# Performance work log

Measured on AMD Instinct MI355X. Metric: run time of the kernel, lower is better.

Reference implementation:

```python
import jax, jax.numpy as jnp
import numpy as np
import math

B, S, D, H = 4, 1024, 1024, 16
DK = D // H


def setup_inputs() -> dict:
    key = jax.random.key(0)
    ks = jax.random.split(key, 14)
    inp = {
        "query": jax.random.normal(ks[0], (B, S, D), dtype=jnp.float32),
        "key": jax.random.normal(ks[1], (B, S, D), dtype=jnp.float32),
        "value": jax.random.normal(ks[2], (B, S, D), dtype=jnp.float32),
        "attention_bias": jax.random.normal(ks[3], (B, S, S, H), dtype=jnp.float32),
        "mask": jax.random.randint(ks[4], (B, S), 0, 2).astype(bool),
    }
    scale = 0.02
    inp["Wq"] = jax.random.normal(ks[5], (D, D), dtype=jnp.float32) * scale
    inp["bq"] = jnp.zeros((D,), dtype=jnp.float32)
    inp["Wk"] = jax.random.normal(ks[6], (D, D), dtype=jnp.float32) * scale
    inp["bk"] = jnp.zeros((D,), dtype=jnp.float32)
    inp["Wv"] = jax.random.normal(ks[7], (D, D), dtype=jnp.float32) * scale
    inp["bv"] = jnp.zeros((D,), dtype=jnp.float32)
    inp["Wo"] = jax.random.normal(ks[8], (D, D), dtype=jnp.float32) * scale
    inp["bo"] = jnp.zeros((D,), dtype=jnp.float32)
    return inp


def reference(query, key, value, attention_bias, mask, Wq, bq, Wk, bk, Wv, bv, Wo, bo):
    # projections (torch Linear: x @ W.T + b), split heads -> [B,H,S,DK]
    def proj(x, W, b):
        y = x @ W.T + b
        return y.reshape(B, S, H, DK).transpose(0, 2, 1, 3)

    q = proj(query, Wq, bq)
    k = proj(key, Wk, bk)
    v = proj(value, Wv, bv)

    bias = attention_bias.transpose(0, 3, 1, 2)  # [B,H,S,S]
    scores = (jnp.einsum("bhqd,bhkd->bhqk", q, k) + bias) / math.sqrt(DK)

    # pairwise mask: outer product of per-token mask, broadcast over heads
    pm = (mask[:, None, :, None] & mask[:, None, None, :])  # [B,1,S,S]
    scores = jnp.where(pm, scores, jnp.float32(-1e9))

    p_attn = jax.nn.softmax(scores, axis=-1)  # dropout is identity in eval
    x = jnp.einsum("bhqk,bhkd->bhqd", p_attn, v)
    x = x.transpose(0, 2, 1, 3).reshape(B, S, D)
    return x @ Wo.T + bo
```

## Files before the change

### kernel.cpp

```cpp
#include <hip/hip_runtime.h>
#include <hip/hip_bf16.h>
#include <math.h>

#define B_ 4
#define S_ 1024
#define D_ 1024
#define H_ 16
#define DK_ 64

typedef short bf16x8 __attribute__((ext_vector_type(8)));
typedef float f32x4 __attribute__((ext_vector_type(4)));

#define MFMA(a, b, c) __builtin_amdgcn_mfma_f32_16x16x32_bf16(a, b, c, 0, 0, 0)

#define GLDS(gp, lp)                                                        \
    __builtin_amdgcn_global_load_lds(                                       \
        (const __attribute__((address_space(1))) void*)(const void*)(gp),   \
        (__attribute__((address_space(3))) void*)(void*)(lp), 16, 0, 0)

static __device__ __forceinline__ unsigned short f2bf(float f) {
    __hip_bfloat16 h = __float2bfloat16(f);
    return *reinterpret_cast<unsigned short*>(&h);
}
static __device__ __forceinline__ float bf2f(unsigned short u) {
    unsigned int x = ((unsigned int)u) << 16;
    union { unsigned int i; float f; } c; c.i = x; return c.f;
}

__global__ __launch_bounds__(256) void cvt_all(
    const float* __restrict__ a, const float* __restrict__ b, const float* __restrict__ c,
    const float* __restrict__ wa, const float* __restrict__ wb,
    const float* __restrict__ wc, const float* __restrict__ wd,
    unsigned short* __restrict__ oa, unsigned short* __restrict__ ob, unsigned short* __restrict__ oc,
    unsigned short* __restrict__ owa, unsigned short* __restrict__ owb,
    unsigned short* __restrict__ owc, unsigned short* __restrict__ owd)
{
    int bx = blockIdx.x;
    const float* in; unsigned short* out; int i;
    if (bx < 12288) {
        int which = bx >> 12;
        in  = which == 0 ? a : which == 1 ? b : c;
        out = which == 0 ? oa : which == 1 ? ob : oc;
        i = (bx & 4095) * 256 + threadIdx.x;
    } else {
        int b2 = bx - 12288;
        int which = b2 >> 10;
        in  = which == 0 ? wa : which == 1 ? wb : which == 2 ? wc : wd;
        out = which == 0 ? owa : which == 1 ? owb : which == 2 ? owc : owd;
        i = (b2 & 1023) * 256 + threadIdx.x;
    }
    float4 v = ((const float4*)in)[i];
    ushort4 o;
    o.x = f2bf(v.x); o.y = f2bf(v.y); o.z = f2bf(v.z); o.w = f2bf(v.w);
    ((ushort4*)out)[i] = o;
}

__global__ __launch_bounds__(256) void prep_bias(
    const float* __restrict__ bias, const int* __restrict__ mask,
    unsigned short* __restrict__ biasP)
{
    const int t = threadIdx.x;
    const int h = t & 15, u = t >> 4;
    const int x = blockIdx.x;
    const int kt = x & 15, q16 = (x >> 4) & 63, b = x >> 10;

    const unsigned short NEG = f2bf(-28672.f);

    int mk[4];
    #pragma unroll
    for (int j = 0; j < 4; ++j) mk[j] = mask[b * 1024 + kt * 64 + j * 16 + u];

    const float* bb = bias + (((size_t)(b * 1024 + q16 * 16) * 1024) + kt * 64) * 16 + h;
    unsigned short* ob = biasP + ((((size_t)(b * 16 + h) * 64 + q16) * 16 + kt) * 64) * 16;

    #pragma unroll
    for (int quad = 0; quad < 4; ++quad) {
        bf16x8 v0, v1;
        #pragma unroll
        for (int r = 0; r < 4; ++r) {
            int q = quad * 4 + r;
            int mq = mask[b * 1024 + q16 * 16 + q];
            #pragma unroll
            for (int j = 0; j < 4; ++j) {
                float v = bb[((size_t)q * 1024 + j * 16 + u) * 16];
                unsigned short pv = (mq && mk[j]) ? f2bf(v * 0.125f) : NEG;
                if (j < 2) v0[j * 4 + r] = (short)pv;
                else       v1[(j - 2) * 4 + r] = (short)pv;
            }
        }
        unsigned short* dst = ob + (size_t)(quad * 16 + u) * 16;
        *(bf16x8*)(dst) = v0;
        *(bf16x8*)(dst + 8) = v1;
    }
}

__global__ __launch_bounds__(256, 2) void gemm128(
    const unsigned short* __restrict__ X0, const unsigned short* __restrict__ X1,
    const unsigned short* __restrict__ X2,
    const unsigned short* __restrict__ W0, const unsigned short* __restrict__ W1,
    const unsigned short* __restrict__ W2,
    const float* __restrict__ bv0, const float* __restrict__ bv1,
    const float* __restrict__ bv2,
    unsigned short* __restrict__ Y0, unsigned short* __restrict__ Y1,
    unsigned short* __restrict__ Y2,
    const int* __restrict__ mask)
{
    __shared__ unsigned short As[128 * 32];
    __shared__ unsigned short Bs[128 * 32];

    const int z = blockIdx.z;
    const unsigned short* X = z == 0 ? X0 : z == 1 ? X1 : X2;
    const unsigned short* W = z == 0 ? W0 : z == 1 ? W1 : W2;
    const float* bvec = z == 0 ? bv0 : z == 1 ? bv1 : bv2;
    unsigned short* Y = z == 0 ? Y0 : z == 1 ? Y1 : Y2;

    const int t = threadIdx.x;
    const int w = t >> 6, l = t & 63;
    const int lane16 = l & 15, quad = l >> 4;
    const int m0 = blockIdx.y * 128, n0 = blockIdx.x * 128;
    const int wr = w >> 1, wc = w & 1;

    const int srow = w * 16 + (l >> 2);
    const unsigned short* agp = X + (size_t)(m0 + srow) * 1024 + (l & 3) * 8;
    const unsigned short* bgp = W + (size_t)(n0 + srow) * 1024 + (l & 3) * 8;
    unsigned short* alp = As + w * 512 + l * 8;
    unsigned short* blp = Bs + w * 512 + l * 8;

    f32x4 zero = {0.f, 0.f, 0.f, 0.f};
    f32x4 acc[4][4];
    #pragma unroll
    for (int i = 0; i < 4; ++i)
        #pragma unroll
        for (int j = 0; j < 4; ++j) acc[i][j] = zero;

    for (int kt = 0; kt < 1024; kt += 32) {
        GLDS(agp + kt, alp);
        GLDS(agp + kt + 64 * 1024, alp + 2048);
        GLDS(bgp + kt, blp);
        GLDS(bgp + kt + 64 * 1024, blp + 2048);
        __syncthreads();

        bf16x8 af[4], bfv[4];
        #pragma unroll
        for (int i = 0; i < 4; ++i)
            af[i] = *(const bf16x8*)(As + (wr * 64 + i * 16 + lane16) * 32 + quad * 8);
        #pragma unroll
        for (int j = 0; j < 4; ++j)
            bfv[j] = *(const bf16x8*)(Bs + (wc * 64 + j * 16 + lane16) * 32 + quad * 8);

        #pragma unroll
        for (int i = 0; i < 4; ++i)
            #pragma unroll
            for (int j = 0; j < 4; ++j)
                acc[i][j] = MFMA(af[i], bfv[j], acc[i][j]);
        __syncthreads();
    }

    float bvl[4];
    #pragma unroll
    for (int j = 0; j < 4; ++j) bvl[j] = bvec[n0 + wc * 64 + j * 16 + lane16];

    if (z == 2) {
        const int bb = m0 >> 10;
        const int sb = (m0 & 1023) + wr * 64;
        #pragma unroll
        for (int i = 0; i < 4; ++i) {
            #pragma unroll
            for (int j = 0; j < 4; ++j) {
                int n = n0 + wc * 64 + j * 16 + lane16;
                ushort4 pk;
                pk.x = f2bf(acc[i][j][0] + bvl[j]);
                pk.y = f2bf(acc[i][j][1] + bvl[j]);
                pk.z = f2bf(acc[i][j][2] + bvl[j]);
                pk.w = f2bf(acc[i][j][3] + bvl[j]);
                int s = sb + i * 16 + quad * 4;
                *(ushort4*)(Y + ((size_t)(bb * 1024 + n)) * 1024 + s) = pk;
            }
        }
    } else {
        #pragma unroll
        for (int i = 0; i < 4; ++i) {
            int mrow[4];
            #pragma unroll
            for (int r = 0; r < 4; ++r)
                mrow[r] = (z == 0) ? mask[m0 + wr * 64 + i * 16 + quad * 4 + r] : 1;
            #pragma unroll
            for (int j = 0; j < 4; ++j) {
                int n = n0 + wc * 64 + j * 16 + lane16;
                #pragma unroll
                for (int r = 0; r < 4; ++r) {
                    size_t m = m0 + wr * 64 + i * 16 + quad * 4 + r;
                    float val = acc[i][j][r] + bvl[j];
                    if (z == 0) val = mrow[r] ? val * 0.125f : 0.f;
                    Y[m * 1024 + n] = f2bf(val);
                }
            }
        }
    }
}

__global__ __launch_bounds__(256, 2) void attn_mfma(
    const unsigned short* __restrict__ Qp, const unsigned short* __restrict__ Kp,
    const unsigned short* __restrict__ VpT, const unsigned short* __restrict__ biasP,
    unsigned short* __restrict__ Xp)
{
    __shared__ unsigned short Ks[2][64 * 64];
    __shared__ unsigned short Vs[2][64 * 64];
    __shared__ unsigned short Ps[4][16 * 64];

    const int t = threadIdx.x;
    const int w = t >> 6, l = t & 63;
    const int lane16 = l & 15, quad = l >> 4;

    const int bid = blockIdx.x;
    const int bh = bid & 63, qt = bid >> 6;
    const int h = bh & 15, b = bh >> 4;
    const int qrow0 = qt * 64 + w * 16;
    const int q16 = qt * 4 + w;

    bf16x8 qf[2];
    #pragma unroll
    for (int c = 0; c < 2; ++c)
        qf[c] = *(const bf16x8*)(Qp + (size_t)(b * 1024 + qrow0 + lane16) * 1024
                                 + h * 64 + c * 32 + quad * 8);

    bf16x8 ones;
    #pragma unroll
    for (int e = 0; e < 8; ++e) ones[e] = (short)0x3F80;

    const unsigned short* bp = biasP
        + ((((size_t)(b * 16 + h) * 64 + q16) * 16) * 64 + l) * 16;

    const int krow = w * 8 + (l >> 3);
    const int kgran = (l & 7) ^ ((l >> 3) & 7);
    const unsigned short* kg = Kp + (size_t)(b * 1024 + krow) * 1024 + h * 64 + kgran * 8;
    const unsigned short* vg = VpT + ((size_t)(b * 16 + h) * 64 + krow) * 1024 + kgran * 8;
    unsigned short* kst = &Ks[0][w * 512 + l * 8];
    unsigned short* vst = &Vs[0][w * 512 + l * 8];

    GLDS(kg, kst);
    GLDS(kg + (size_t)32 * 1024, kst + 32 * 64);
    GLDS(vg, vst);
    GLDS(vg + (size_t)32 * 1024, vst + 32 * 64);
    bf16x8 bfr0 = *(const bf16x8*)(bp);
    bf16x8 bfr1 = *(const bf16x8*)(bp + 8);

    f32x4 zero = {0.f, 0.f, 0.f, 0.f};
    f32x4 o[4];
    #pragma unroll
    for (int j = 0; j < 4; ++j) o[j] = zero;
    float m_i[4] = {-1e30f, -1e30f, -1e30f, -1e30f};
    float l_i[4] = {0.f, 0.f, 0.f, 0.f};

    char* psb = (char*)&Ps[w][0];

    for (int kt16 = 0; kt16 < 16; ++kt16) {
        const int cur = kt16 & 1;
        __syncthreads();

        if (kt16 < 15) {
            const size_t kn = (size_t)(kt16 + 1) * 64;
            unsigned short* kd = kst + (cur ^ 1) * 4096;
            unsigned short* vd = vst + (cur ^ 1) * 4096;
            GLDS(kg + kn * 1024, kd);
            GLDS(kg + (kn + 32) * 1024, kd + 32 * 64);
            GLDS(vg + kn, vd);
            GLDS(vg + kn + (size_t)32 * 1024, vd + 32 * 64);
        }

        const unsigned short* Kc = &Ks[0][0] + cur * 4096;
        const unsigned short* Vc = &Vs[0][0] + cur * 4096;

        f32x4 s[4];
        #pragma unroll
        for (int j = 0; j < 2; ++j)
            #pragma unroll
            for (int r = 0; r < 4; ++r) {
                s[j][r]     = bf2f((unsigned short)bfr0[j * 4 + r]);
                s[2 + j][r] = bf2f((unsigned short)bfr1[j * 4 + r]);
            }

        __builtin_amdgcn_s_setprio(1);
        #pragma unroll
        for (int j = 0; j < 4; ++j) {
            #pragma unroll
            for (int c = 0; c < 2; ++c) {
                bf16x8 kf = *(const bf16x8*)(Kc + (j * 16 + lane16) * 64
                                             + (((c * 4 + quad) ^ (lane16 & 7)) * 8));
                s[j] = MFMA(qf[c], kf, s[j]);
            }
        }
        __builtin_amdgcn_s_setprio(0);

        if (kt16 < 15) {
            bfr0 = *(const bf16x8*)(bp + (size_t)(kt16 + 1) * 1024);
            bfr1 = *(const bf16x8*)(bp + (size_t)(kt16 + 1) * 1024 + 8);
        }

        float p[4][4];
        float alpha_r[4];
        #pragma unroll
        for (int r = 0; r < 4; ++r) {
            float mx = fmaxf(fmaxf(s[0][r], s[1][r]), fmaxf(s[2][r], s[3][r]));
            #pragma unroll
            for (int d = 1; d < 16; d <<= 1) mx = fmaxf(mx, __shfl_xor(mx, d, 64));
            float mnew = fmaxf(m_i[r], mx);
            float alpha = __expf(m_i[r] - mnew);
            m_i[r] = mnew;
            alpha_r[r] = alpha;
            #pragma unroll
            for (int j = 0; j < 4; ++j) p[j][r] = __expf(s[j][r] - mnew);
            #pragma unroll
            for (int jd = 0; jd < 4; ++jd) o[jd][r] *= alpha;
        }

        #pragma unroll
        for (int j = 0; j < 4; ++j)
            #pragma unroll
            for (int r = 0; r < 4; ++r) {
                int row = quad * 4 + r;
                int cb = (j * 16 + lane16) * 2;
                *(unsigned short*)(psb + row * 128 + (cb ^ ((row & 7) << 4))) = f2bf(p[j][r]);
            }
        asm volatile("" ::: "memory");

        bf16x8 pf[2];
        #pragma unroll
        for (int c = 0; c < 2; ++c) {
            int cb = c * 64 + quad * 16;
            pf[c] = *(const bf16x8*)(psb + lane16 * 128 + (cb ^ ((lane16 & 7) << 4)));
        }

        f32x4 lacc = zero;
        __builtin_amdgcn_s_setprio(1);
        #pragma unroll
        for (int jd = 0; jd < 4; ++jd)
            #pragma unroll
            for (int c = 0; c < 2; ++c) {
                bf16x8 vf = *(const bf16x8*)(Vc + (jd * 16 + lane16) * 64
                                             + (((c * 4 + quad) ^ (lane16 & 7)) * 8));
                o[jd] = MFMA(pf[c], vf, o[jd]);
            }
        #pragma unroll
        for (int c = 0; c < 2; ++c)
            lacc = MFMA(pf[c], ones, lacc);
        __builtin_amdgcn_s_setprio(0);

        #pragma unroll
        for (int r = 0; r < 4; ++r)
            l_i[r] = l_i[r] * alpha_r[r] + lacc[r];
    }

    float inv[4];
    #pragma unroll
    for (int r = 0; r < 4; ++r) inv[r] = 1.0f / l_i[r];

    #pragma unroll
    for (int jd = 0; jd < 4; ++jd)
        #pragma unroll
        for (int r = 0; r < 4; ++r)
            Xp[(size_t)(b * 1024 + qrow0 + quad * 4 + r) * 1024
               + h * 64 + jd * 16 + lane16] = f2bf(o[jd][r] * inv[r]);
}

__global__ __launch_bounds__(256, 2) void gemm_o64(
    const unsigned short* __restrict__ X, const unsigned short* __restrict__ W,
    const float* __restrict__ bvec, float* __restrict__ Y)
{
    __shared__ unsigned short As[128 * 32];
    __shared__ unsigned short Bs[64 * 32];

    const int t = threadIdx.x;
    const int w = t >> 6, l = t & 63;
    const int lane16 = l & 15, quad = l >> 4;
    const int m0 = blockIdx.y * 128, n0 = blockIdx.x * 64;
    const int wr = w >> 1, wc = w & 1;

    const int srow = w * 16 + (l >> 2);
    const unsigned short* agp = X + (size_t)(m0 + srow) * 1024 + (l & 3) * 8;
    const unsigned short* bgp = W + (size_t)(n0 + srow) * 1024 + (l & 3) * 8;
    unsigned short* alp = As + w * 512 + l * 8;
    unsigned short* blp = Bs + w * 512 + l * 8;

    f32x4 zero = {0.f, 0.f, 0.f, 0.f};
    f32x4 acc[4][2];
    #pragma unroll
    for (int i = 0; i < 4; ++i)
        #pragma unroll
        for (int j = 0; j < 2; ++j) acc[i][j] = zero;

    for (int kt = 0; kt < 1024; kt += 32) {
        GLDS(agp + kt, alp);
        GLDS(agp + kt + 64 * 1024, alp + 2048);
        GLDS(bgp + kt, blp);
        __syncthreads();

        bf16x8 af[4], bfv[2];
        #pragma unroll
        for (int i = 0; i < 4; ++i)
            af[i] = *(const bf16x8*)(As + (wr * 64 + i * 16 + lane16) * 32 + quad * 8);
        #pragma unroll
        for (int j = 0; j < 2; ++j)
            bfv[j] = *(const bf16x8*)(Bs + (wc * 32 + j * 16 + lane16) * 32 + quad * 8);

        #pragma unroll
        for (int i = 0; i < 4; ++i)
            #pragma unroll
            for (int j = 0; j < 2; ++j)
                acc[i][j] = MFMA(af[i], bfv[j], acc[i][j]);
        __syncthreads();
    }

    float bvl[2];
    #pragma unroll
    for (int j = 0; j < 2; ++j) bvl[j] = bvec[n0 + wc * 32 + j * 16 + lane16];

    #pragma unroll
    for (int i = 0; i < 4; ++i)
        #pragma unroll
        for (int j = 0; j < 2; ++j) {
            int n = n0 + wc * 32 + j * 16 + lane16;
            #pragma unroll
            for (int r = 0; r < 4; ++r) {
                size_t m = m0 + wr * 64 + i * 16 + quad * 4 + r;
                Y[m * 1024 + n] = acc[i][j][r] + bvl[j];
            }
        }
}

extern "C" void kernel_launch(void* const* d_in, const int* in_sizes, int n_in,
                              void* d_out, int out_size, void* d_ws, size_t ws_size,
                              hipStream_t stream)
{
    const float* query = (const float*)d_in[0];
    const float* key   = (const float*)d_in[1];
    const float* value = (const float*)d_in[2];
    const float* abias = (const float*)d_in[3];
    const int*   mask  = (const int*)d_in[4];
    const float* Wq = (const float*)d_in[5];
    const float* bq = (const float*)d_in[6];
    const float* Wk = (const float*)d_in[7];
    const float* bk = (const float*)d_in[8];
    const float* Wv = (const float*)d_in[9];
    const float* bv = (const float*)d_in[10];
    const float* Wo = (const float*)d_in[11];
    const float* bo = (const float*)d_in[12];
    float* out = (float*)d_out;

    const size_t T = (size_t)B_ * S_ * D_;
    const size_t WSZ = (size_t)D_ * D_;
    const size_t BPSZ = (size_t)B_ * H_ * S_ * S_;
    unsigned short* p = (unsigned short*)d_ws;
    unsigned short* biasP = p;  p += BPSZ;
    unsigned short* qb  = p;  p += T;
    unsigned short* kb  = p;  p += T;
    unsigned short* vb  = p;  p += T;
    unsigned short* wqb = p;  p += WSZ;
    unsigned short* wkb = p;  p += WSZ;
    unsigned short* wvb = p;  p += WSZ;
    unsigned short* wob = p;  p += WSZ;
    unsigned short* Qpj = p;  p += T;
    unsigned short* Kpj = p;  p += T;
    unsigned short* VpT = p;  p += T;
    unsigned short* Xpj = p;  p += T;

    cvt_all<<<dim3(16384), 256, 0, stream>>>(
        query, key, value, Wq, Wk, Wv, Wo,
        qb, kb, vb, wqb, wkb, wvb, wob);

    prep_bias<<<dim3(4096), 256, 0, stream>>>(abias, mask, biasP);

    gemm128<<<dim3(8, 32, 3), 256, 0, stream>>>(
        qb, kb, vb, wqb, wkb, wvb, bq, bk, bv,
        Qpj, Kpj, VpT, mask);

    attn_mfma<<<dim3(1024), 256, 0, stream>>>(Qpj, Kpj, VpT, biasP, Xpj);

    gemm_o64<<<dim3(16, 32), 256, 0, stream>>>(Xpj, wob, bo, out);
}
```

Before: 561.4 us.

## Fuse bias/mask preprocessing into attention kernel, reading fp32 bias directly

Removes the prep_bias kernel and its bf16 permuted bias buffer. The attention kernel now reads the raw fp32 [B,S,S,H] bias and the mask itself, applying the scale and mask in registers. The block index mapping is reordered so that the 16 heads sharing a bias cache line run in blocks far apart, with the q-tile index varying fastest. This saves a full write and re-read of the bias intermediate. In exchange, the strided fp32 loads (stride 16 floats across heads) are uncoalesced and are issued synchronously inside the loop rather than prefetched.

```diff
diff --git a/kernel.cpp b/kernel.cpp
--- a/kernel.cpp
+++ b/kernel.cpp
@@ -21,10 +21,6 @@
 static __device__ __forceinline__ unsigned short f2bf(float f) {
     __hip_bfloat16 h = __float2bfloat16(f);
     return *reinterpret_cast<unsigned short*>(&h);
-}
-static __device__ __forceinline__ float bf2f(unsigned short u) {
-    unsigned int x = ((unsigned int)u) << 16;
-    union { unsigned int i; float f; } c; c.i = x; return c.f;
 }
 
 __global__ __launch_bounds__(256) void cvt_all(
@@ -55,45 +51,6 @@
     ((ushort4*)out)[i] = o;
 }
 
-__global__ __launch_bounds__(256) void prep_bias(
-    const float* __restrict__ bias, const int* __restrict__ mask,
-    unsigned short* __restrict__ biasP)
-{
-    const int t = threadIdx.x;
-    const int h = t & 15, u = t >> 4;
-    const int x = blockIdx.x;
-    const int kt = x & 15, q16 = (x >> 4) & 63, b = x >> 10;
-
-    const unsigned short NEG = f2bf(-28672.f);
-
-    int mk[4];
-    #pragma unroll
-    for (int j = 0; j < 4; ++j) mk[j] = mask[b * 1024 + kt * 64 + j * 16 + u];
-
-    const float* bb = bias + (((size_t)(b * 1024 + q16 * 16) * 1024) + kt * 64) * 16 + h;
-    unsigned short* ob = biasP + ((((size_t)(b * 16 + h) * 64 + q16) * 16 + kt) * 64) * 16;
-
-    #pragma unroll
-    for (int quad = 0; quad < 4; ++quad) {
-        bf16x8 v0, v1;
-        #pragma unroll
-        for (int r = 0; r < 4; ++r) {
-            int q = quad * 4 + r;
-            int mq = mask[b * 1024 + q16 * 16 + q];
-            #pragma unroll
-            for (int j = 0; j < 4; ++j) {
-                float v = bb[((size_t)q * 1024 + j * 16 + u) * 16];
-                unsigned short pv = (mq && mk[j]) ? f2bf(v * 0.125f) : NEG;
-                if (j < 2) v0[j * 4 + r] = (short)pv;
-                else       v1[(j - 2) * 4 + r] = (short)pv;
-            }
-        }
-        unsigned short* dst = ob + (size_t)(quad * 16 + u) * 16;
-        *(bf16x8*)(dst) = v0;
-        *(bf16x8*)(dst + 8) = v1;
-    }
-}
-
 __global__ __launch_bounds__(256, 2) void gemm128(
     const unsigned short* __restrict__ X0, const unsigned short* __restrict__ X1,
     const unsigned short* __restrict__ X2,
@@ -201,8 +158,8 @@
 
 __global__ __launch_bounds__(256, 2) void attn_mfma(
     const unsigned short* __restrict__ Qp, const unsigned short* __restrict__ Kp,
-    const unsigned short* __restrict__ VpT, const unsigned short* __restrict__ biasP,
-    unsigned short* __restrict__ Xp)
+    const unsigned short* __restrict__ VpT, const float* __restrict__ bias,
+    const int* __restrict__ mask, unsigned short* __restrict__ Xp)
 {
     __shared__ unsigned short Ks[2][64 * 64];
     __shared__ unsigned short Vs[2][64 * 64];
@@ -213,10 +170,12 @@
     const int lane16 = l & 15, quad = l >> 4;
 
     const int bid = blockIdx.x;
-    const int bh = bid & 63, qt = bid >> 6;
-    const int h = bh & 15, b = bh >> 4;
+    const int h = bid >> 6;
+    const int b = (bid >> 4) & 3;
+    const int qt = bid & 15;
     const int qrow0 = qt * 64 + w * 16;
-    const int q16 = qt * 4 + w;
+
+    const float NEGF = -28672.f;
 
     bf16x8 qf[2];
     #pragma unroll
@@ -228,8 +187,11 @@
     #pragma unroll
     for (int e = 0; e < 8; ++e) ones[e] = (short)0x3F80;
 
-    const unsigned short* bp = biasP
-        + ((((size_t)(b * 16 + h) * 64 + q16) * 16) * 64 + l) * 16;
+    int mq[4];
+    #pragma unroll
+    for (int r = 0; r < 4; ++r) mq[r] = mask[b * 1024 + qrow0 + quad * 4 + r];
+
+    const float* bt = bias + ((size_t)(b * 1024 + qrow0 + quad * 4) * 1024 + lane16) * 16 + h;
 
     const int krow = w * 8 + (l >> 3);
     const int kgran = (l & 7) ^ ((l >> 3) & 7);
@@ -242,8 +204,6 @@
     GLDS(kg + (size_t)32 * 1024, kst + 32 * 64);
     GLDS(vg, vst);
     GLDS(vg + (size_t)32 * 1024, vst + 32 * 64);
-    bf16x8 bfr0 = *(const bf16x8*)(bp);
-    bf16x8 bfr1 = *(const bf16x8*)(bp + 8);
 
     f32x4 zero = {0.f, 0.f, 0.f, 0.f};
     f32x4 o[4];
@@ -257,6 +217,17 @@
     for (int kt16 = 0; kt16 < 16; ++kt16) {
         const int cur = kt16 & 1;
         __syncthreads();
+
+        int mk[4];
+        #pragma unroll
+        for (int j = 0; j < 4; ++j)
+            mk[j] = mask[b * 1024 + kt16 * 64 + j * 16 + lane16];
+        float bfv[4][4];
+        #pragma unroll
+        for (int j = 0; j < 4; ++j)
+            #pragma unroll
+            for (int r = 0; r < 4; ++r)
+                bfv[j][r] = bt[(size_t)r * 16384 + j * 256];
 
         if (kt16 < 15) {
             const size_t kn = (size_t)(kt16 + 1) * 64;
@@ -271,14 +242,14 @@
         const unsigned short* Kc = &Ks[0][0] + cur * 4096;
         const unsigned short* Vc = &Vs[0][0] + cur * 4096;
 
+        float mkadd[4];
+        #pragma unroll
+        for (int j = 0; j < 4; ++j) mkadd[j] = mk[j] ? 0.f : NEGF;
         f32x4 s[4];
         #pragma unroll
-        for (int j = 0; j < 2; ++j)
-            #pragma unroll
-            for (int r = 0; r < 4; ++r) {
-                s[j][r]     = bf2f((unsigned short)bfr0[j * 4 + r]);
-                s[2 + j][r] = bf2f((unsigned short)bfr1[j * 4 + r]);
-            }
+        for (int j = 0; j < 4; ++j)
+            #pragma unroll
+            for (int r = 0; r < 4; ++r) s[j][r] = mkadd[j];
 
         __builtin_amdgcn_s_setprio(1);
         #pragma unroll
@@ -292,10 +263,13 @@
         }
         __builtin_amdgcn_s_setprio(0);
 
-        if (kt16 < 15) {
-            bfr0 = *(const bf16x8*)(bp + (size_t)(kt16 + 1) * 1024);
-            bfr1 = *(const bf16x8*)(bp + (size_t)(kt16 + 1) * 1024 + 8);
-        }
+        #pragma unroll
+        for (int j = 0; j < 4; ++j)
+            #pragma unroll
+            for (int r = 0; r < 4; ++r) {
+                float v = fmaf(bfv[j][r], 0.125f, s[j][r]);
+                s[j][r] = mq[r] ? v : NEGF;
+            }
 
         float p[4][4];
         float alpha_r[4];
@@ -349,6 +323,8 @@
         #pragma unroll
         for (int r = 0; r < 4; ++r)
             l_i[r] = l_i[r] * alpha_r[r] + lacc[r];
+
+        bt += 1024;
     }
 
     float inv[4];
@@ -449,9 +425,7 @@
 
     const size_t T = (size_t)B_ * S_ * D_;
     const size_t WSZ = (size_t)D_ * D_;
-    const size_t BPSZ = (size_t)B_ * H_ * S_ * S_;
     unsigned short* p = (unsigned short*)d_ws;
-    unsigned short* biasP = p;  p += BPSZ;
     unsigned short* qb  = p;  p += T;
     unsigned short* kb  = p;  p += T;
     unsigned short* vb  = p;  p += T;
@@ -468,13 +442,11 @@
         query, key, value, Wq, Wk, Wv, Wo,
         qb, kb, vb, wqb, wkb, wvb, wob);
 
-    prep_bias<<<dim3(4096), 256, 0, stream>>>(abias, mask, biasP);
-
     gemm128<<<dim3(8, 32, 3), 256, 0, stream>>>(
         qb, kb, vb, wqb, wkb, wvb, bq, bk, bv,
         Qpj, Kpj, VpT, mask);
 
-    attn_mfma<<<dim3(1024), 256, 0, stream>>>(Qpj, Kpj, VpT, biasP, Xpj);
+    attn_mfma<<<dim3(1024), 256, 0, stream>>>(Qpj, Kpj, VpT, abias, mask, Xpj);
 
     gemm_o64<<<dim3(16, 32), 256, 0, stream>>>(Xpj, wob, bo, out);
 }
```

New measurement: 671.0 us. 1.2x slower.

## Process two 16-row query tiles per wave in attention kernel

Applied to the files above, without the earlier changes.

Each wave now handles 32 query rows (two 16-row sub-tiles) instead of 16, so every block covers 128 queries and the grid is halved to 512 blocks. Each K/V fragment read from shared memory feeds two MFMAs, which halves K/V global and LDS traffic per query row. The cost is roughly doubled accumulator, score and bias registers per thread, plus a larger P buffer in shared memory. That can lower occupancy, and 512 blocks on the device's CUs gives less parallelism for hiding latency.

```diff
diff --git a/kernel.cpp b/kernel.cpp
--- a/kernel.cpp
+++ b/kernel.cpp
@@ -206,30 +206,33 @@
 {
     __shared__ unsigned short Ks[2][64 * 64];
     __shared__ unsigned short Vs[2][64 * 64];
-    __shared__ unsigned short Ps[4][16 * 64];
+    __shared__ unsigned short Ps[4][2][16 * 64];
 
     const int t = threadIdx.x;
     const int w = t >> 6, l = t & 63;
     const int lane16 = l & 15, quad = l >> 4;
 
     const int bid = blockIdx.x;
-    const int bh = bid & 63, qt = bid >> 6;
+    const int bh = bid & 63, qt2 = bid >> 6;
     const int h = bh & 15, b = bh >> 4;
-    const int qrow0 = qt * 64 + w * 16;
-    const int q16 = qt * 4 + w;
-
-    bf16x8 qf[2];
-    #pragma unroll
-    for (int c = 0; c < 2; ++c)
-        qf[c] = *(const bf16x8*)(Qp + (size_t)(b * 1024 + qrow0 + lane16) * 1024
-                                 + h * 64 + c * 32 + quad * 8);
+    const int qrow0 = qt2 * 128 + w * 32;
+
+    bf16x8 qf[2][2];
+    #pragma unroll
+    for (int i = 0; i < 2; ++i)
+        #pragma unroll
+        for (int c = 0; c < 2; ++c)
+            qf[i][c] = *(const bf16x8*)(Qp + (size_t)(b * 1024 + qrow0 + i * 16 + lane16) * 1024
+                                        + h * 64 + c * 32 + quad * 8);
 
     bf16x8 ones;
     #pragma unroll
     for (int e = 0; e < 8; ++e) ones[e] = (short)0x3F80;
 
-    const unsigned short* bp = biasP
-        + ((((size_t)(b * 16 + h) * 64 + q16) * 16) * 64 + l) * 16;
+    const unsigned short* bp[2];
+    #pragma unroll
+    for (int i = 0; i < 2; ++i)
+        bp[i] = biasP + ((((size_t)(b * 16 + h) * 64 + (qt2 * 8 + w * 2 + i)) * 16) * 64 + l) * 16;
 
     const int krow = w * 8 + (l >> 3);
     const int kgran = (l & 7) ^ ((l >> 3) & 7);
@@ -242,17 +245,24 @@
     GLDS(kg + (size_t)32 * 1024, kst + 32 * 64);
     GLDS(vg, vst);
     GLDS(vg + (size_t)32 * 1024, vst + 32 * 64);
-    bf16x8 bfr0 = *(const bf16x8*)(bp);
-    bf16x8 bfr1 = *(const bf16x8*)(bp + 8);
+    bf16x8 bfr[2][2];
+    #pragma unroll
+    for (int i = 0; i < 2; ++i) {
+        bfr[i][0] = *(const bf16x8*)(bp[i]);
+        bfr[i][1] = *(const bf16x8*)(bp[i] + 8);
+    }
 
     f32x4 zero = {0.f, 0.f, 0.f, 0.f};
-    f32x4 o[4];
-    #pragma unroll
-    for (int j = 0; j < 4; ++j) o[j] = zero;
-    float m_i[4] = {-1e30f, -1e30f, -1e30f, -1e30f};
-    float l_i[4] = {0.f, 0.f, 0.f, 0.f};
-
-    char* psb = (char*)&Ps[w][0];
+    f32x4 o[2][4];
+    #pragma unroll
+    for (int i = 0; i < 2; ++i)
+        #pragma unroll
+        for (int j = 0; j < 4; ++j) o[i][j] = zero;
+    float m_i[2][4], l_i[2][4];
+    #pragma unroll
+    for (int i = 0; i < 2; ++i)
+        #pragma unroll
+        for (int r = 0; r < 4; ++r) { m_i[i][r] = -1e30f; l_i[i][r] = 0.f; }
 
     for (int kt16 = 0; kt16 < 16; ++kt16) {
         const int cur = kt16 & 1;
@@ -271,14 +281,16 @@
         const unsigned short* Kc = &Ks[0][0] + cur * 4096;
         const unsigned short* Vc = &Vs[0][0] + cur * 4096;
 
-        f32x4 s[4];
-        #pragma unroll
-        for (int j = 0; j < 2; ++j)
-            #pragma unroll
-            for (int r = 0; r < 4; ++r) {
-                s[j][r]     = bf2f((unsigned short)bfr0[j * 4 + r]);
-                s[2 + j][r] = bf2f((unsigned short)bfr1[j * 4 + r]);
-            }
+        f32x4 s[2][4];
+        #pragma unroll
+        for (int i = 0; i < 2; ++i)
+            #pragma unroll
+            for (int j = 0; j < 2; ++j)
+                #pragma unroll
+                for (int r = 0; r < 4; ++r) {
+                    s[i][j][r]     = bf2f((unsigned short)bfr[i][0][j * 4 + r]);
+                    s[i][2 + j][r] = bf2f((unsigned short)bfr[i][1][j * 4 + r]);
+                }
 
         __builtin_amdgcn_s_setprio(1);
         #pragma unroll
@@ -287,51 +299,66 @@
             for (int c = 0; c < 2; ++c) {
                 bf16x8 kf = *(const bf16x8*)(Kc + (j * 16 + lane16) * 64
                                              + (((c * 4 + quad) ^ (lane16 & 7)) * 8));
-                s[j] = MFMA(qf[c], kf, s[j]);
+                #pragma unroll
+                for (int i = 0; i < 2; ++i)
+                    s[i][j] = MFMA(qf[i][c], kf, s[i][j]);
             }
         }
         __builtin_amdgcn_s_setprio(0);
 
         if (kt16 < 15) {
-            bfr0 = *(const bf16x8*)(bp + (size_t)(kt16 + 1) * 1024);
-            bfr1 = *(const bf16x8*)(bp + (size_t)(kt16 + 1) * 1024 + 8);
-        }
-
-        float p[4][4];
-        float alpha_r[4];
-        #pragma unroll
-        for (int r = 0; r < 4; ++r) {
-            float mx = fmaxf(fmaxf(s[0][r], s[1][r]), fmaxf(s[2][r], s[3][r]));
-            #pragma unroll
-            for (int d = 1; d < 16; d <<= 1) mx = fmaxf(mx, __shfl_xor(mx, d, 64));
-            float mnew = fmaxf(m_i[r], mx);
-            float alpha = __expf(m_i[r] - mnew);
-            m_i[r] = mnew;
-            alpha_r[r] = alpha;
-            #pragma unroll
-            for (int j = 0; j < 4; ++j) p[j][r] = __expf(s[j][r] - mnew);
-            #pragma unroll
-            for (int jd = 0; jd < 4; ++jd) o[jd][r] *= alpha;
-        }
-
-        #pragma unroll
-        for (int j = 0; j < 4; ++j)
+            #pragma unroll
+            for (int i = 0; i < 2; ++i) {
+                bfr[i][0] = *(const bf16x8*)(bp[i] + (size_t)(kt16 + 1) * 1024);
+                bfr[i][1] = *(const bf16x8*)(bp[i] + (size_t)(kt16 + 1) * 1024 + 8);
+            }
+        }
+
+        float p[2][4][4];
+        float alpha_r[2][4];
+        #pragma unroll
+        for (int i = 0; i < 2; ++i)
             #pragma unroll
             for (int r = 0; r < 4; ++r) {
-                int row = quad * 4 + r;
-                int cb = (j * 16 + lane16) * 2;
-                *(unsigned short*)(psb + row * 128 + (cb ^ ((row & 7) << 4))) = f2bf(p[j][r]);
-            }
+                float mx = fmaxf(fmaxf(s[i][0][r], s[i][1][r]), fmaxf(s[i][2][r], s[i][3][r]));
+                #pragma unroll
+                for (int d = 1; d < 16; d <<= 1) mx = fmaxf(mx, __shfl_xor(mx, d, 64));
+                float mnew = fmaxf(m_i[i][r], mx);
+                float alpha = __expf(m_i[i][r] - mnew);
+                m_i[i][r] = mnew;
+                alpha_r[i][r] = alpha;
+                #pragma unroll
+                for (int j = 0; j < 4; ++j) p[i][j][r] = __expf(s[i][j][r] - mnew);
+                #pragma unroll
+                for (int jd = 0; jd < 4; ++jd) o[i][jd][r] *= alpha;
+            }
+
+        #pragma unroll
+        for (int i = 0; i < 2; ++i) {
+            char* psb = (char*)&Ps[w][i][0];
+            #pragma unroll
+            for (int j = 0; j < 4; ++j)
+                #pragma unroll
+                for (int r = 0; r < 4; ++r) {
+                    int row = quad * 4 + r;
+                    int cb = (j * 16 + lane16) * 2;
+                    *(unsigned short*)(psb + row * 128 + (cb ^ ((row & 7) << 4))) = f2bf(p[i][j][r]);
+                }
+        }
         asm volatile("" ::: "memory");
 
-        bf16x8 pf[2];
-        #pragma unroll
-        for (int c = 0; c < 2; ++c) {
-            int cb = c * 64 + quad * 16;
-            pf[c] = *(const bf16x8*)(psb + lane16 * 128 + (cb ^ ((lane16 & 7) << 4)));
-        }
-
-        f32x4 lacc = zero;
+        bf16x8 pf[2][2];
+        #pragma unroll
+        for (int i = 0; i < 2; ++i) {
+            char* psb = (char*)&Ps[w][i][0];
+            #pragma unroll
+            for (int c = 0; c < 2; ++c) {
+                int cb = c * 64 + quad * 16;
+                pf[i][c] = *(const bf16x8*)(psb + lane16 * 128 + (cb ^ ((lane16 & 7) << 4)));
+            }
+        }
+
+        f32x4 lacc[2] = {zero, zero};
         __builtin_amdgcn_s_setprio(1);
         #pragma unroll
         for (int jd = 0; jd < 4; ++jd)
@@ -339,28 +366,36 @@
             for (int c = 0; c < 2; ++c) {
                 bf16x8 vf = *(const bf16x8*)(Vc + (jd * 16 + lane16) * 64
                                              + (((c * 4 + quad) ^ (lane16 & 7)) * 8));
-                o[jd] = MFMA(pf[c], vf, o[jd]);
-            }
-        #pragma unroll
-        for (int c = 0; c < 2; ++c)
-            lacc = MFMA(pf[c], ones, lacc);
+                #pragma unroll
+                for (int i = 0; i < 2; ++i)
+                    o[i][jd] = MFMA(pf[i][c], vf, o[i][jd]);
+            }
+        #pragma unroll
+        for (int i = 0; i < 2; ++i)
+            #pragma unroll
+            for (int c = 0; c < 2; ++c)
+                lacc[i] = MFMA(pf[i][c], ones, lacc[i]);
         __builtin_amdgcn_s_setprio(0);
 
         #pragma unroll
-        for (int r = 0; r < 4; ++r)
-            l_i[r] = l_i[r] * alpha_r[r] + lacc[r];
-    }
-
-    float inv[4];
-    #pragma unroll
-    for (int r = 0; r < 4; ++r) inv[r] = 1.0f / l_i[r];
-
-    #pragma unroll
-    for (int jd = 0; jd < 4; ++jd)
-        #pragma unroll
-        for (int r = 0; r < 4; ++r)
-            Xp[(size_t)(b * 1024 + qrow0 + quad * 4 + r) * 1024
-               + h * 64 + jd * 16 + lane16] = f2bf(o[jd][r] * inv[r]);
+        for (int i = 0; i < 2; ++i)
+            #pragma unroll
+            for (int r = 0; r < 4; ++r)
+                l_i[i][r] = l_i[i][r] * alpha_r[i][r] + lacc[i][r];
+    }
+
+    #pragma unroll
+    for (int i = 0; i < 2; ++i) {
+        float inv[4];
+        #pragma unroll
+        for (int r = 0; r < 4; ++r) inv[r] = 1.0f / l_i[i][r];
+        #pragma unroll
+        for (int jd = 0; jd < 4; ++jd)
+            #pragma unroll
+            for (int r = 0; r < 4; ++r)
+                Xp[(size_t)(b * 1024 + qrow0 + i * 16 + quad * 4 + r) * 1024
+                   + h * 64 + jd * 16 + lane16] = f2bf(o[i][jd][r] * inv[r]);
+    }
 }
 
 __global__ __launch_bounds__(256, 2) void gemm_o64(
@@ -474,7 +509,7 @@
         qb, kb, vb, wqb, wkb, wvb, bq, bk, bv,
         Qpj, Kpj, VpT, mask);
 
-    attn_mfma<<<dim3(1024), 256, 0, stream>>>(Qpj, Kpj, VpT, biasP, Xpj);
+    attn_mfma<<<dim3(512), 256, 0, stream>>>(Qpj, Kpj, VpT, biasP, Xpj);
 
     gemm_o64<<<dim3(16, 32), 256, 0, stream>>>(Xpj, wob, bo, out);
 }
```

Measured after the change: 559.6 us. Within noise of the previous version (-0.3%).
